# Kernel tuning notes

Measured on AMD Instinct MI355X. Metric: run time of the kernel, lower is better.

Reference implementation:

```python
import jax, jax.numpy as jnp
import numpy as np

EMB = 1024
HEADS = 16
HEAD_DIM = EMB // HEADS
B, S = 4, 2048


def setup_inputs() -> dict:
    key = jax.random.key(0)
    ks = jax.random.split(key, 9)
    sc = 1.0 / np.sqrt(EMB)
    x = jax.random.normal(ks[0], (B, S, EMB), dtype=jnp.float32)
    Wq = jax.random.normal(ks[1], (EMB, EMB), dtype=jnp.float32) * sc
    bq = jax.random.normal(ks[2], (EMB,), dtype=jnp.float32) * 0.02
    Wk = jax.random.normal(ks[3], (EMB, EMB), dtype=jnp.float32) * sc
    bk = jax.random.normal(ks[4], (EMB,), dtype=jnp.float32) * 0.02
    Wv = jax.random.normal(ks[5], (EMB, EMB), dtype=jnp.float32) * sc
    bv = jax.random.normal(ks[6], (EMB,), dtype=jnp.float32) * 0.02
    Wo = jax.random.normal(ks[7], (EMB, EMB), dtype=jnp.float32) * sc
    bo = jax.random.normal(ks[8], (EMB,), dtype=jnp.float32) * 0.02
    # causal mask: 1 where allowed (lower triangular), 0 elsewhere
    causal_mask = jnp.tril(jnp.ones((S, S), dtype=jnp.int32))[None, None]
    return {"x": x, "Wq": Wq, "bq": bq, "Wk": Wk, "bk": bk,
            "Wv": Wv, "bv": bv, "Wo": Wo, "bo": bo,
            "causal_mask": causal_mask}


def reference(x, Wq, bq, Wk, bk, Wv, bv, Wo, bo, causal_mask):
    bs, seq, _ = x.shape
    # nn.Linear: x @ W.T + b; then view [bs, seq, H, hd] and transpose to [bs, H, seq, hd]
    def proj(W, b):
        return (x @ W.T + b).reshape(bs, seq, HEADS, HEAD_DIM).transpose(0, 2, 1, 3)
    q, k, v = proj(Wq, bq), proj(Wk, bk), proj(Wv, bv)
    scale = 1.0 / np.sqrt(HEAD_DIM).astype(np.float32)
    dots = jnp.einsum('bhqd,bhkd->bhqk', q, k) * scale  # [B, H, S, S]
    dots = jnp.where(causal_mask == 0, -jnp.inf, dots)
    attn = jax.nn.softmax(dots, axis=-1)
    out = jnp.einsum('bhqk,bhkd->bhqd', attn, v)  # [B, H, S, hd]
    out = out.transpose(0, 2, 1, 3).reshape(bs, seq, EMB)
    return out @ Wo.T + bo
```

## Files before the change

### kernel.cpp

```cpp
#include <hip/hip_runtime.h>
#include <hip/hip_bf16.h>

typedef __attribute__((ext_vector_type(8))) short short8;
typedef __attribute__((ext_vector_type(4))) float floatx4;

#define B_    4
#define S_    2048
#define EMB_  1024
#define NH_   16
#define HD_   64

#if __has_builtin(__builtin_amdgcn_exp2f)
#define EXP2F(x) __builtin_amdgcn_exp2f(x)
#else
#define EXP2F(x) exp2f(x)
#endif

__device__ __forceinline__ void async_cp16(const void* g, void* l) {
  __builtin_amdgcn_global_load_lds(
      (const __attribute__((address_space(1))) unsigned int*)g,
      (__attribute__((address_space(3))) unsigned int*)l, 16, 0, 0);
}

__device__ __forceinline__ ushort4 cvt4(const float4 f) {
  __bf16 t[4] = {(__bf16)f.x, (__bf16)f.y, (__bf16)f.z, (__bf16)f.w};
  return *(const ushort4*)t;
}

__global__ __launch_bounds__(256)
void cvt_kernel(const float* __restrict__ x,
                const float* __restrict__ wq, const float* __restrict__ wk,
                const float* __restrict__ wv, const float* __restrict__ wo,
                const float* __restrict__ bq, const float* __restrict__ bk,
                const float* __restrict__ bv,
                __bf16* __restrict__ xb, __bf16* __restrict__ Wcat,
                __bf16* __restrict__ Wob, float* __restrict__ bcat)
{
  const int NX4 = 2097152;
  const int NW4 = 262144;
  int g = blockIdx.x * 256 + threadIdx.x;
  if (g < NX4) {
    *(ushort4*)(xb + (size_t)g * 4) = cvt4(*(const float4*)(x + (size_t)g * 4));
    return;
  }
  g -= NX4;
  if (g < 3 * NW4) {
    const float* src = (g < NW4) ? wq : (g < 2 * NW4) ? wk : wv;
    const int gg = (g < NW4) ? g : (g < 2 * NW4) ? g - NW4 : g - 2 * NW4;
    *(ushort4*)(Wcat + (size_t)g * 4) = cvt4(*(const float4*)(src + (size_t)gg * 4));
    return;
  }
  g -= 3 * NW4;
  if (g < NW4) {
    *(ushort4*)(Wob + (size_t)g * 4) = cvt4(*(const float4*)(wo + (size_t)g * 4));
    return;
  }
  g -= NW4;
  if (g < 768) {
    const float* src = (g < 256) ? bq : (g < 512) ? bk : bv;
    *(float4*)(bcat + (size_t)g * 4) = *(const float4*)(src + (size_t)(g & 255) * 4);
  }
}

__global__ __launch_bounds__(256)
void gemm_qkv_kernel(const __bf16* __restrict__ A, const __bf16* __restrict__ W,
                     const float* __restrict__ bcat,
                     __bf16* __restrict__ Qb, __bf16* __restrict__ Kb,
                     __bf16* __restrict__ Vb)
{
  __shared__ __attribute__((aligned(16))) __bf16 As[128 * 32];
  __shared__ __attribute__((aligned(16))) __bf16 Ws[128 * 32];
  const int tid  = threadIdx.x;
  const int wave = tid >> 6, lane = tid & 63;
  const int l15  = lane & 15, quad = lane >> 4;
  const int wm   = wave >> 1, wn = wave & 1;
  const int bm   = blockIdx.y * 128;
  const int bn   = blockIdx.x * 128;
  const int widx = bn >> 10;
  const float QS = 0.180336880f;

  floatx4 acc[4][4];
#pragma unroll
  for (int i = 0; i < 4; ++i)
#pragma unroll
    for (int j = 0; j < 4; ++j) acc[i][j] = (floatx4){0.f, 0.f, 0.f, 0.f};

  const int srow = tid >> 2;
  const int scol = (tid & 3) << 3;
  const __bf16* Ag = A + (size_t)(bm + srow) * 1024 + scol;
  const __bf16* Wg = W + (size_t)(bn + srow) * 1024 + scol;
  __bf16* AsD = As + tid * 8;
  __bf16* WsD = Ws + tid * 8;

  for (int k0 = 0; k0 < 1024; k0 += 32) {
    __syncthreads();
    async_cp16(Ag + k0,             AsD);
    async_cp16(Ag + k0 + 64 * 1024, AsD + 2048);
    async_cp16(Wg + k0,             WsD);
    async_cp16(Wg + k0 + 64 * 1024, WsD + 2048);
    __syncthreads();
    short8 af[4], wf[4];
#pragma unroll
    for (int mi = 0; mi < 4; ++mi)
      af[mi] = *(const short8*)(As + ((wm * 64 + mi * 16 + l15) << 5) + (quad << 3));
#pragma unroll
    for (int ni = 0; ni < 4; ++ni)
      wf[ni] = *(const short8*)(Ws + ((wn * 64 + ni * 16 + l15) << 5) + (quad << 3));
#pragma unroll
    for (int mi = 0; mi < 4; ++mi)
#pragma unroll
      for (int ni = 0; ni < 4; ++ni)
        acc[mi][ni] = __builtin_amdgcn_mfma_f32_16x16x32_bf16(af[mi], wf[ni], acc[mi][ni], 0, 0, 0);
  }

#pragma unroll
  for (int ni = 0; ni < 4; ++ni) {
    const int n  = bn + wn * 64 + ni * 16 + l15;
    const float bvb = bcat[n];
    const int np = n & 1023;
    const int h = np >> 6, d = np & 63;
#pragma unroll
    for (int mi = 0; mi < 4; ++mi) {
      const int m0 = bm + wm * 64 + mi * 16 + quad * 4;
      const int b = m0 >> 11, s0 = m0 & 2047;
      floatx4 v = acc[mi][ni];
      if (widx == 0) {
        const size_t base = (size_t)(b * 16 + h) * (S_ * 64) + d;
#pragma unroll
        for (int r = 0; r < 4; ++r)
          Qb[base + (size_t)(s0 + r) * 64] = (__bf16)((v[r] + bvb) * QS);
      } else if (widx == 1) {
        const size_t base = (size_t)(b * 16 + h) * (S_ * 64) + d;
#pragma unroll
        for (int r = 0; r < 4; ++r)
          Kb[base + (size_t)(s0 + r) * 64] = (__bf16)(v[r] + bvb);
      } else {
        const size_t base = ((size_t)(b * 16 + h) * 64 + d) * S_ + s0;
        union { ushort4 u4; unsigned short u[4]; } pk;
#pragma unroll
        for (int r = 0; r < 4; ++r) {
          __bf16 hv = (__bf16)(v[r] + bvb);
          pk.u[r] = *(unsigned short*)&hv;
        }
        *(ushort4*)(Vb + base) = pk.u4;
      }
    }
  }
}

__global__ __launch_bounds__(256, 4)
void attn_kernel(__bf16* __restrict__ Q, const __bf16* __restrict__ K,
                 const __bf16* __restrict__ Vt)
{
  __shared__ __attribute__((aligned(16))) __bf16 Ks[64 * 72];
  __shared__ __attribute__((aligned(16))) __bf16 Vs[80 * 72];
  __shared__ __attribute__((aligned(16))) __bf16 Ps[4][16 * 72];

  const int tid  = threadIdx.x;
  const int wave = tid >> 6, lane = tid & 63;
  const int l15  = lane & 15, quad = lane >> 4;
  const int qtA  = blockIdx.x, bh = blockIdx.y;
  const size_t hb = (size_t)bh * (S_ * 64);
  const float MASKV = -1.0e30f;

  for (int idx = tid; idx < 16 * 72; idx += 256)
    Vs[64 * 72 + idx] = (idx < 72) ? (__bf16)1.0f : (__bf16)0.0f;

  for (int qsel = 0; qsel < 2; ++qsel) {
    const int qt = qsel ? (31 - qtA) : qtA;
    const int q0 = qt * 64;
    const int qw = q0 + wave * 16;

    short8 aq[2];
#pragma unroll
    for (int kk = 0; kk < 2; ++kk)
      aq[kk] = *(const short8*)(Q + hb + (size_t)(qw + l15) * 64 + kk * 32 + quad * 8);

    floatx4 oacc[4];
#pragma unroll
    for (int j = 0; j < 4; ++j) oacc[j] = (floatx4){0.f, 0.f, 0.f, 0.f};
    floatx4 lacc = (floatx4){0.f, 0.f, 0.f, 0.f};
    float mst[4];
#pragma unroll
    for (int r = 0; r < 4; ++r) mst[r] = MASKV;

    for (int kt = 0; kt <= qt; ++kt) {
      __syncthreads();
      {
        const int r = tid >> 3;
        const int c = (tid & 7) << 3;
#pragma unroll
        for (int p = 0; p < 2; ++p) {
          const int row = r + p * 32;
          *(uint4*)(&Ks[row * 72 + c]) = *(const uint4*)(K  + hb + (size_t)(kt * 64 + row) * 64 + c);
          *(uint4*)(&Vs[row * 72 + c]) = *(const uint4*)(Vt + hb + (size_t)row * S_ + kt * 64 + c);
        }
      }
      __syncthreads();

      floatx4 sacc[4];
#pragma unroll
      for (int j = 0; j < 4; ++j) sacc[j] = (floatx4){0.f, 0.f, 0.f, 0.f};
#pragma unroll
      for (int kk = 0; kk < 2; ++kk) {
        short8 bk[4];
#pragma unroll
        for (int ni = 0; ni < 4; ++ni)
          bk[ni] = *(const short8*)(&Ks[(ni * 16 + l15) * 72 + kk * 32 + quad * 8]);
#pragma unroll
        for (int ni = 0; ni < 4; ++ni)
          sacc[ni] = __builtin_amdgcn_mfma_f32_16x16x32_bf16(aq[kk], bk[ni], sacc[ni], 0, 0, 0);
      }

      const bool needmask = (kt == qt);
      const int sc0 = kt * 64 + l15;
#pragma unroll
      for (int r = 0; r < 4; ++r) {
        const int qg = qw + quad * 4 + r;
        float z[4];
        if (needmask) {
#pragma unroll
          for (int ni = 0; ni < 4; ++ni) {
            float zz = sacc[ni][r];
            if (sc0 + ni * 16 > qg) zz = MASKV;
            z[ni] = zz;
          }
        } else {
#pragma unroll
          for (int ni = 0; ni < 4; ++ni) z[ni] = sacc[ni][r];
        }
        float tmax = fmaxf(fmaxf(z[0], z[1]), fmaxf(z[2], z[3]));
        tmax = fmaxf(tmax, __shfl_xor(tmax, 1));
        tmax = fmaxf(tmax, __shfl_xor(tmax, 2));
        tmax = fmaxf(tmax, __shfl_xor(tmax, 4));
        tmax = fmaxf(tmax, __shfl_xor(tmax, 8));
        const float mold = mst[r];
        const float mnew = fmaxf(mold, tmax);
        mst[r] = mnew;
        const float alpha = EXP2F(mold - mnew);
#pragma unroll
        for (int ni = 0; ni < 4; ++ni) {
          const float p = EXP2F(z[ni] - mnew);
          Ps[wave][(quad * 4 + r) * 72 + ni * 16 + l15] = (__bf16)p;
        }
#pragma unroll
        for (int ni = 0; ni < 4; ++ni) oacc[ni][r] *= alpha;
        lacc[r] *= alpha;
      }

      __syncthreads();

#pragma unroll
      for (int kk = 0; kk < 2; ++kk) {
        const short8 ap = *(const short8*)(&Ps[wave][l15 * 72 + kk * 32 + quad * 8]);
        short8 bv[4];
#pragma unroll
        for (int ni = 0; ni < 4; ++ni)
          bv[ni] = *(const short8*)(&Vs[(ni * 16 + l15) * 72 + kk * 32 + quad * 8]);
        const short8 bl = *(const short8*)(&Vs[(64 + l15) * 72 + kk * 32 + quad * 8]);
#pragma unroll
        for (int ni = 0; ni < 4; ++ni)
          oacc[ni] = __builtin_amdgcn_mfma_f32_16x16x32_bf16(ap, bv[ni], oacc[ni], 0, 0, 0);
        lacc = __builtin_amdgcn_mfma_f32_16x16x32_bf16(ap, bl, lacc, 0, 0, 0);
      }
    }

#pragma unroll
    for (int r = 0; r < 4; ++r) {
      const float lv  = __shfl(lacc[r], lane & 48);
      const float inv = 1.0f / fmaxf(lv, 1e-20f);
      const int qg = qw + quad * 4 + r;
      const size_t rowb = hb + (size_t)qg * 64;
#pragma unroll
      for (int ni = 0; ni < 4; ++ni)
        Q[rowb + ni * 16 + l15] = (__bf16)(oacc[ni][r] * inv);
    }
  }
}

__global__ __launch_bounds__(256)
void gemm_o_kernel(const __bf16* __restrict__ A, const __bf16* __restrict__ W,
                   const float* __restrict__ bias, float* __restrict__ out)
{
  __shared__ __attribute__((aligned(16))) __bf16 As[128 * 32];
  __shared__ __attribute__((aligned(16))) __bf16 Ws[128 * 32];
  const int tid  = threadIdx.x;
  const int wave = tid >> 6, lane = tid & 63;
  const int l15  = lane & 15, quad = lane >> 4;
  const int wm   = wave >> 1, wn = wave & 1;
  const int bm   = blockIdx.y * 128;
  const int bn   = blockIdx.x * 128;

  floatx4 acc[4][4];
#pragma unroll
  for (int i = 0; i < 4; ++i)
#pragma unroll
    for (int j = 0; j < 4; ++j) acc[i][j] = (floatx4){0.f, 0.f, 0.f, 0.f};

  const int srow = tid >> 2;
  const int scol = (tid & 3) << 3;
  const __bf16* Wg = W + (size_t)(bn + srow) * 1024 + scol;
  const int bb = bm >> 11;
  const int ss = (bm & 2047) + srow;
  __bf16* AsD = As + tid * 8;
  __bf16* WsD = Ws + tid * 8;

  for (int k0 = 0; k0 < 1024; k0 += 32) {
    const int c = k0 + scol, h = c >> 6, dd = c & 63;
    const __bf16* pa0 = A + (((size_t)(bb * 16 + h) * S_) + ss) * 64 + dd;
    __syncthreads();
    async_cp16(pa0,           AsD);
    async_cp16(pa0 + 64 * 64, AsD + 2048);
    async_cp16(Wg + k0,             WsD);
    async_cp16(Wg + k0 + 64 * 1024, WsD + 2048);
    __syncthreads();

    short8 af[4], wf[4];
#pragma unroll
    for (int mi = 0; mi < 4; ++mi)
      af[mi] = *(const short8*)(As + ((wm * 64 + mi * 16 + l15) << 5) + (quad << 3));
#pragma unroll
    for (int ni = 0; ni < 4; ++ni)
      wf[ni] = *(const short8*)(Ws + ((wn * 64 + ni * 16 + l15) << 5) + (quad << 3));
#pragma unroll
    for (int mi = 0; mi < 4; ++mi)
#pragma unroll
      for (int ni = 0; ni < 4; ++ni)
        acc[mi][ni] = __builtin_amdgcn_mfma_f32_16x16x32_bf16(af[mi], wf[ni], acc[mi][ni], 0, 0, 0);
  }

#pragma unroll
  for (int ni = 0; ni < 4; ++ni) {
    const int n = bn + wn * 64 + ni * 16 + l15;
    const float bvb = bias[n];
#pragma unroll
    for (int mi = 0; mi < 4; ++mi) {
      const int m0 = bm + wm * 64 + mi * 16 + quad * 4;
      floatx4 v = acc[mi][ni];
#pragma unroll
      for (int r = 0; r < 4; ++r)
        out[(size_t)(m0 + r) * 1024 + n] = v[r] + bvb;
    }
  }
}

extern "C" void kernel_launch(void* const* d_in, const int* in_sizes, int n_in,
                              void* d_out, int out_size, void* d_ws, size_t ws_size,
                              hipStream_t stream) {
  const float* x  = (const float*)d_in[0];
  const float* Wq = (const float*)d_in[1];
  const float* bq = (const float*)d_in[2];
  const float* Wk = (const float*)d_in[3];
  const float* bk = (const float*)d_in[4];
  const float* Wv = (const float*)d_in[5];
  const float* bv = (const float*)d_in[6];
  const float* Wo = (const float*)d_in[7];
  const float* bo = (const float*)d_in[8];

  const size_t BUF = (size_t)B_ * NH_ * S_ * HD_;
  __bf16* ws   = (__bf16*)d_ws;
  __bf16* xb   = ws;
  __bf16* Wcat = ws + 8388608;
  __bf16* Wob  = ws + 11534336;
  __bf16* Qb   = ws + 12582912;
  float*  bcat = (float*)(ws + 20971520);
  __bf16* Kb   = (__bf16*)d_out;
  __bf16* Vb   = (__bf16*)d_out + BUF;

  dim3 blk(256);
  cvt_kernel<<<12291, blk, 0, stream>>>(x, Wq, Wk, Wv, Wo, bq, bk, bv,
                                        xb, Wcat, Wob, bcat);
  gemm_qkv_kernel<<<dim3(24, 64), blk, 0, stream>>>(xb, Wcat, bcat, Qb, Kb, Vb);
  attn_kernel<<<dim3(16, 64), blk, 0, stream>>>(Qb, Kb, Vb);
  gemm_o_kernel<<<dim3(8, 64), blk, 0, stream>>>(Qb, Wob, bo, (float*)d_out);
}
```

Measured before the change: 309.1 us.

## Transpose attention MFMA layout, prefetch K/V in registers, drop ones-column rowsum

Swaps the MFMA operand order so each lane owns one query row, which lets the row max use two cross-lane shuffles instead of four and the row sum be accumulated in scalar registers. This removes the extra ones-column MFMA used to compute the softmax denominator. Next-tile K/V loads are issued into registers before the current tile's compute, to hide global latency. The block-wide barrier before PV is replaced by a wave-local LDS waitcnt, and P and O are written as packed 4-element vectors. Register pressure rises from the prefetch buffers.

```diff
diff --git a/kernel.cpp b/kernel.cpp
--- a/kernel.cpp
+++ b/kernel.cpp
@@ -153,7 +153,7 @@
                  const __bf16* __restrict__ Vt)
 {
   __shared__ __attribute__((aligned(16))) __bf16 Ks[64 * 72];
-  __shared__ __attribute__((aligned(16))) __bf16 Vs[80 * 72];
+  __shared__ __attribute__((aligned(16))) __bf16 Vs[64 * 72];
   __shared__ __attribute__((aligned(16))) __bf16 Ps[4][16 * 72];
 
   const int tid  = threadIdx.x;
@@ -163,40 +163,51 @@
   const size_t hb = (size_t)bh * (S_ * 64);
   const float MASKV = -1.0e30f;
 
-  for (int idx = tid; idx < 16 * 72; idx += 256)
-    Vs[64 * 72 + idx] = (idx < 72) ? (__bf16)1.0f : (__bf16)0.0f;
+  const int srow = tid >> 3;
+  const int scol = (tid & 7) << 3;
 
   for (int qsel = 0; qsel < 2; ++qsel) {
     const int qt = qsel ? (31 - qtA) : qtA;
-    const int q0 = qt * 64;
-    const int qw = q0 + wave * 16;
+    const int qw = qt * 64 + wave * 16;
+    const int myq = qw + l15;
 
     short8 aq[2];
 #pragma unroll
     for (int kk = 0; kk < 2; ++kk)
-      aq[kk] = *(const short8*)(Q + hb + (size_t)(qw + l15) * 64 + kk * 32 + quad * 8);
+      aq[kk] = *(const short8*)(Q + hb + (size_t)myq * 64 + kk * 32 + quad * 8);
 
     floatx4 oacc[4];
 #pragma unroll
     for (int j = 0; j < 4; ++j) oacc[j] = (floatx4){0.f, 0.f, 0.f, 0.f};
-    floatx4 lacc = (floatx4){0.f, 0.f, 0.f, 0.f};
-    float mst[4];
-#pragma unroll
-    for (int r = 0; r < 4; ++r) mst[r] = MASKV;
+    float lsum = 0.0f;
+    float mrun = MASKV;
+
+    uint4 kreg0, kreg1, vreg0, vreg1;
+    {
+      const __bf16* kp = K  + hb + (size_t)srow * 64 + scol;
+      const __bf16* vp = Vt + hb + (size_t)srow * S_ + scol;
+      kreg0 = *(const uint4*)kp;
+      kreg1 = *(const uint4*)(kp + 32 * 64);
+      vreg0 = *(const uint4*)vp;
+      vreg1 = *(const uint4*)(vp + (size_t)32 * S_);
+    }
 
     for (int kt = 0; kt <= qt; ++kt) {
       __syncthreads();
-      {
-        const int r = tid >> 3;
-        const int c = (tid & 7) << 3;
-#pragma unroll
-        for (int p = 0; p < 2; ++p) {
-          const int row = r + p * 32;
-          *(uint4*)(&Ks[row * 72 + c]) = *(const uint4*)(K  + hb + (size_t)(kt * 64 + row) * 64 + c);
-          *(uint4*)(&Vs[row * 72 + c]) = *(const uint4*)(Vt + hb + (size_t)row * S_ + kt * 64 + c);
-        }
-      }
+      *(uint4*)(&Ks[srow * 72 + scol])        = kreg0;
+      *(uint4*)(&Ks[(srow + 32) * 72 + scol]) = kreg1;
+      *(uint4*)(&Vs[srow * 72 + scol])        = vreg0;
+      *(uint4*)(&Vs[(srow + 32) * 72 + scol]) = vreg1;
       __syncthreads();
+
+      if (kt < qt) {
+        const __bf16* kp = K  + hb + (size_t)((kt + 1) * 64 + srow) * 64 + scol;
+        const __bf16* vp = Vt + hb + (size_t)srow * S_ + (kt + 1) * 64 + scol;
+        kreg0 = *(const uint4*)kp;
+        kreg1 = *(const uint4*)(kp + 32 * 64);
+        vreg0 = *(const uint4*)vp;
+        vreg1 = *(const uint4*)(vp + (size_t)32 * S_);
+      }
 
       floatx4 sacc[4];
 #pragma unroll
@@ -209,71 +220,77 @@
           bk[ni] = *(const short8*)(&Ks[(ni * 16 + l15) * 72 + kk * 32 + quad * 8]);
 #pragma unroll
         for (int ni = 0; ni < 4; ++ni)
-          sacc[ni] = __builtin_amdgcn_mfma_f32_16x16x32_bf16(aq[kk], bk[ni], sacc[ni], 0, 0, 0);
-      }
-
-      const bool needmask = (kt == qt);
-      const int sc0 = kt * 64 + l15;
-#pragma unroll
-      for (int r = 0; r < 4; ++r) {
-        const int qg = qw + quad * 4 + r;
-        float z[4];
-        if (needmask) {
-#pragma unroll
-          for (int ni = 0; ni < 4; ++ni) {
-            float zz = sacc[ni][r];
-            if (sc0 + ni * 16 > qg) zz = MASKV;
-            z[ni] = zz;
-          }
-        } else {
-#pragma unroll
-          for (int ni = 0; ni < 4; ++ni) z[ni] = sacc[ni][r];
-        }
-        float tmax = fmaxf(fmaxf(z[0], z[1]), fmaxf(z[2], z[3]));
-        tmax = fmaxf(tmax, __shfl_xor(tmax, 1));
-        tmax = fmaxf(tmax, __shfl_xor(tmax, 2));
-        tmax = fmaxf(tmax, __shfl_xor(tmax, 4));
-        tmax = fmaxf(tmax, __shfl_xor(tmax, 8));
-        const float mold = mst[r];
-        const float mnew = fmaxf(mold, tmax);
-        mst[r] = mnew;
-        const float alpha = EXP2F(mold - mnew);
-#pragma unroll
-        for (int ni = 0; ni < 4; ++ni) {
-          const float p = EXP2F(z[ni] - mnew);
-          Ps[wave][(quad * 4 + r) * 72 + ni * 16 + l15] = (__bf16)p;
-        }
-#pragma unroll
-        for (int ni = 0; ni < 4; ++ni) oacc[ni][r] *= alpha;
-        lacc[r] *= alpha;
-      }
-
-      __syncthreads();
+          sacc[ni] = __builtin_amdgcn_mfma_f32_16x16x32_bf16(bk[ni], aq[kk], sacc[ni], 0, 0, 0);
+      }
+
+      if (kt == qt) {
+        const int kb = kt * 64 + quad * 4;
+#pragma unroll
+        for (int ni = 0; ni < 4; ++ni)
+#pragma unroll
+          for (int r = 0; r < 4; ++r)
+            if (kb + ni * 16 + r > myq) sacc[ni][r] = MASKV;
+      }
+
+      float t0 = fmaxf(fmaxf(sacc[0][0], sacc[0][1]), fmaxf(sacc[0][2], sacc[0][3]));
+      float t1 = fmaxf(fmaxf(sacc[1][0], sacc[1][1]), fmaxf(sacc[1][2], sacc[1][3]));
+      float t2 = fmaxf(fmaxf(sacc[2][0], sacc[2][1]), fmaxf(sacc[2][2], sacc[2][3]));
+      float t3 = fmaxf(fmaxf(sacc[3][0], sacc[3][1]), fmaxf(sacc[3][2], sacc[3][3]));
+      float tmax = fmaxf(fmaxf(t0, t1), fmaxf(t2, t3));
+      tmax = fmaxf(tmax, __shfl_xor(tmax, 16));
+      tmax = fmaxf(tmax, __shfl_xor(tmax, 32));
+
+      const float mold = mrun;
+      const float mnew = fmaxf(mold, tmax);
+      mrun = mnew;
+      const float alpha = EXP2F(mold - mnew);
+
+      float psum = 0.0f;
+#pragma unroll
+      for (int ni = 0; ni < 4; ++ni) {
+        float4 p;
+        p.x = EXP2F(sacc[ni][0] - mnew);
+        p.y = EXP2F(sacc[ni][1] - mnew);
+        p.z = EXP2F(sacc[ni][2] - mnew);
+        p.w = EXP2F(sacc[ni][3] - mnew);
+        psum += (p.x + p.y) + (p.z + p.w);
+        *(ushort4*)(&Ps[wave][l15 * 72 + ni * 16 + quad * 4]) = cvt4(p);
+      }
+      lsum = lsum * alpha + psum;
+#pragma unroll
+      for (int ni = 0; ni < 4; ++ni)
+#pragma unroll
+        for (int r = 0; r < 4; ++r) oacc[ni][r] *= alpha;
+
+      asm volatile("s_waitcnt lgkmcnt(0)" ::: "memory");
+      __builtin_amdgcn_sched_barrier(0);
 
 #pragma unroll
       for (int kk = 0; kk < 2; ++kk) {
-        const short8 ap = *(const short8*)(&Ps[wave][l15 * 72 + kk * 32 + quad * 8]);
+        const short8 pf = *(const short8*)(&Ps[wave][l15 * 72 + kk * 32 + quad * 8]);
         short8 bv[4];
 #pragma unroll
         for (int ni = 0; ni < 4; ++ni)
           bv[ni] = *(const short8*)(&Vs[(ni * 16 + l15) * 72 + kk * 32 + quad * 8]);
-        const short8 bl = *(const short8*)(&Vs[(64 + l15) * 72 + kk * 32 + quad * 8]);
-#pragma unroll
-        for (int ni = 0; ni < 4; ++ni)
-          oacc[ni] = __builtin_amdgcn_mfma_f32_16x16x32_bf16(ap, bv[ni], oacc[ni], 0, 0, 0);
-        lacc = __builtin_amdgcn_mfma_f32_16x16x32_bf16(ap, bl, lacc, 0, 0, 0);
-      }
-    }
-
-#pragma unroll
-    for (int r = 0; r < 4; ++r) {
-      const float lv  = __shfl(lacc[r], lane & 48);
-      const float inv = 1.0f / fmaxf(lv, 1e-20f);
-      const int qg = qw + quad * 4 + r;
-      const size_t rowb = hb + (size_t)qg * 64;
-#pragma unroll
-      for (int ni = 0; ni < 4; ++ni)
-        Q[rowb + ni * 16 + l15] = (__bf16)(oacc[ni][r] * inv);
+#pragma unroll
+        for (int ni = 0; ni < 4; ++ni)
+          oacc[ni] = __builtin_amdgcn_mfma_f32_16x16x32_bf16(bv[ni], pf, oacc[ni], 0, 0, 0);
+      }
+    }
+
+    float l = lsum;
+    l += __shfl_xor(l, 16);
+    l += __shfl_xor(l, 32);
+    const float inv = 1.0f / fmaxf(l, 1e-20f);
+    const size_t rowb = hb + (size_t)myq * 64;
+#pragma unroll
+    for (int ni = 0; ni < 4; ++ni) {
+      float4 o;
+      o.x = oacc[ni][0] * inv;
+      o.y = oacc[ni][1] * inv;
+      o.z = oacc[ni][2] * inv;
+      o.w = oacc[ni][3] * inv;
+      *(ushort4*)(Q + rowb + ni * 16 + quad * 4) = cvt4(o);
     }
   }
 }
```

Result: faster. 291.0 us (-5.8%).
